# Kernel optimization log

Hardware: AMD Instinct MI355X
Metric: run time of the kernel (lower is better)

The kernel has to match this reference:

```python
import jax, jax.numpy as jnp
import numpy as np

B, NPG, F, H, C, DEG = 64, 1024, 128, 128, 10, 16   # graphs, nodes/graph, feat, hidden, classes, degree
N = B * NPG            # 65536 total nodes
E = N * DEG            # 1048576 total edges
K = 820                # ceil(0.8 * 1024) SAGPooling keep count per graph


def _glorot(key, shape):
    lim = float(np.sqrt(6.0 / (shape[0] + shape[1])))
    return jax.random.uniform(key, shape, jnp.float32, -lim, lim)


def setup_inputs() -> dict:
    key = jax.random.key(0)
    ks = jax.random.split(key, 16)
    # edges: endpoints drawn within the same graph
    gid = jnp.repeat(jnp.arange(B, dtype=jnp.int64), NPG * DEG)
    src = gid * NPG + jax.random.randint(ks[0], (E,), 0, NPG, dtype=jnp.int64)
    dst = gid * NPG + jax.random.randint(ks[1], (E,), 0, NPG, dtype=jnp.int64)
    return {
        "x": jax.random.normal(ks[2], (N, F), jnp.float32),
        "src": src,
        "dst": dst,
        # conv1: GraphConv(F, H)  (lin_rel has bias, lin_root has none)
        "W1_rel": _glorot(ks[3], (F, H)), "b1": jnp.zeros((H,), jnp.float32), "W1_root": _glorot(ks[4], (F, H)),
        # convs[0], convs[1]: GraphConv(H, H)
        "W2_rel": _glorot(ks[5], (H, H)), "b2": jnp.zeros((H,), jnp.float32), "W2_root": _glorot(ks[6], (H, H)),
        "W3_rel": _glorot(ks[7], (H, H)), "b3": jnp.zeros((H,), jnp.float32), "W3_root": _glorot(ks[8], (H, H)),
        # SAGPooling score GNN: GraphConv(H, 1)
        "Ws_rel": _glorot(ks[9], (H, 1)), "bs": jnp.zeros((1,), jnp.float32), "Ws_root": _glorot(ks[10], (H, 1)),
        # MLP head
        "Wl1": _glorot(ks[11], (3 * H, H)), "bl1": jnp.zeros((H,), jnp.float32),
        "Wl2": _glorot(ks[12], (H, C)), "bl2": jnp.zeros((C,), jnp.float32),
    }


def _mean_agg(x, src, dst, emask):
    # scatter-mean of source features onto destinations, honoring edge mask
    msg = x[src] * emask[:, None]                                   # [E, d]
    agg = jax.ops.segment_sum(msg, dst, num_segments=N)             # [N, d]
    deg = jax.ops.segment_sum(emask, dst, num_segments=N)           # [N]
    return agg / jnp.maximum(deg, 1.0)[:, None]


def _gconv(x, src, dst, emask, W_rel, b, W_root):
    # PyG GraphConv: lin_rel(mean_j x_j) + lin_root(x)
    return _mean_agg(x, src, dst, emask) @ W_rel + b + x @ W_root


def _gpool(x, nmask):
    # global_mean_pool over valid nodes of each graph
    xm = (x * nmask[:, None]).reshape(B, NPG, -1).sum(axis=1)       # [B, d]
    cnt = nmask.reshape(B, NPG).sum(axis=1)                          # [B]
    return xm / cnt[:, None]


def reference(x, src, dst,
              W1_rel, b1, W1_root, W2_rel, b2, W2_root, W3_rel, b3, W3_root,
              Ws_rel, bs, Ws_root, Wl1, bl1, Wl2, bl2):
    nmask = jnp.ones((N,), x.dtype)
    emask = jnp.ones((E,), x.dtype)

    x = jax.nn.relu(_gconv(x, src, dst, emask, W1_rel, b1, W1_root))
    xs = [_gpool(x, nmask)]

    # convs[0]
    x = jax.nn.relu(_gconv(x, src, dst, emask, W2_rel, b2, W2_root))
    xs.append(_gpool(x, nmask))

    # SAGPooling (ratio=0.8): score via GraphConv(H,1), topk per graph, gate by tanh(score)
    score = _gconv(x, src, dst, emask, Ws_rel, bs, Ws_root)[:, 0]    # [N]
    score_m = jnp.where(nmask > 0, score, -1e30)
    _, idx = jax.lax.top_k(score_m.reshape(B, NPG), K)               # [B, K]
    nmask = jnp.zeros((B, NPG), x.dtype).at[jnp.arange(B)[:, None], idx].set(1.0).reshape(-1)
    x = x * jnp.tanh(score)[:, None] * nmask[:, None]
    emask = emask * nmask[src] * nmask[dst]

    # convs[1]
    x = jax.nn.relu(_gconv(x, src, dst, emask, W3_rel, b3, W3_root))
    xs.append(_gpool(x, nmask))

    h = jnp.concatenate(xs, axis=-1)                                  # [B, 3H] JumpingKnowledge 'cat'
    h = jax.nn.relu(h @ Wl1 + bl1)                                    # dropout: eval mode -> identity
    logits = h @ Wl2 + bl2
    return jax.nn.log_softmax(logits, axis=-1)
```

## Files before the change

### kernel.cpp

```cpp
#include <hip/hip_runtime.h>
#include <hip/hip_bf16.h>

#define NN 65536
#define EE 1048576
#define BG 64
#define NPGC 1024
#define KKEEP 820

typedef unsigned short u16;
typedef unsigned int u32;
typedef __attribute__((ext_vector_type(4))) float f32x4;
typedef __attribute__((ext_vector_type(2))) float f32x2;
typedef __attribute__((ext_vector_type(8))) short bf16x8;

__device__ __forceinline__ float bfu_lo(u32 u) {
    u32 x = u << 16;
    return __builtin_bit_cast(float, x);
}
__device__ __forceinline__ float bfu_hi(u32 u) {
    u32 x = u & 0xffff0000u;
    return __builtin_bit_cast(float, x);
}
__device__ __forceinline__ u16 fbf(float f) {
    __hip_bfloat16 h = __float2bfloat16(f);
    return __builtin_bit_cast(u16, h);
}
__device__ __forceinline__ u32 pack2(float a, float b) {
    return (u32)fbf(a) | ((u32)fbf(b) << 16);
}

__global__ __launch_bounds__(1024) void csr_build_kernel(const int* __restrict__ src,
                                                         const int* __restrict__ dst,
                                                         int* __restrict__ noff,
                                                         int* __restrict__ deg,
                                                         int* __restrict__ csr) {
    __shared__ int hist[NPGC];
    __shared__ int scan[NPGC];
    int g = blockIdx.x, t = threadIdx.x;
    hist[t] = 0;
    __syncthreads();
    int ebase = g * 16384;
    for (int i = t; i < 16384; i += 1024) atomicAdd(&hist[dst[ebase + i] & 1023], 1);
    __syncthreads();
    int d = hist[t];
    scan[t] = d;
    __syncthreads();
    for (int s = 1; s < NPGC; s <<= 1) {
        int add = (t >= s) ? scan[t - s] : 0;
        __syncthreads();
        scan[t] += add;
        __syncthreads();
    }
    int excl = scan[t] - d;
    int node = g * NPGC + t;
    deg[node] = d;
    noff[node] = ebase + excl;
    hist[t] = excl;
    __syncthreads();
    for (int i = t; i < 16384; i += 1024) {
        int dl = dst[ebase + i] & 1023;
        int p = atomicAdd(&hist[dl], 1);
        csr[ebase + p] = src[ebase + i];
    }
}

__global__ void prep_w_kernel(const float* __restrict__ Wr1, const float* __restrict__ Wo1,
                              const float* __restrict__ Wr2, const float* __restrict__ Wo2,
                              const float* __restrict__ Wr3, const float* __restrict__ Wo3,
                              u16* __restrict__ WT) {
    int l = blockIdx.y;
    const float* Wrel = l == 0 ? Wr1 : (l == 1 ? Wr2 : Wr3);
    const float* Wroot = l == 0 ? Wo1 : (l == 1 ? Wo2 : Wo3);
    int idx = blockIdx.x * 256 + threadIdx.x;
    int col = idx >> 7, k = idx & 127;
    float v = (col < 128) ? Wrel[k * 128 + col] : Wroot[k * 128 + (col - 128)];
    WT[l * 32768 + idx] = fbf(v);
}

template <int MODE>
__global__ __launch_bounds__(256, 2) void gemm_kernel(const u16* __restrict__ Xb,
                                                      const float* __restrict__ Xf,
                                                      const float* __restrict__ gate,
                                                      const u16* __restrict__ WT,
                                                      u16* __restrict__ Y) {
    __shared__ u16 As[128][72];
    __shared__ u16 Bs[128][72];
    int rb = blockIdx.x * 128;
    int cb = blockIdx.y * 128;
    int tid = threadIdx.x;
    int lane = tid & 63, wid = tid >> 6;
    int wr = (wid >> 1) << 6, wc = (wid & 1) << 6;
    int lr = lane & 15, lk = (lane >> 4) << 3;
    f32x4 acc[4][4] = {};

    for (int half = 0; half < 2; ++half) {
        int k0 = half << 6;
        if (half) __syncthreads();
        for (int i = tid; i < 1024; i += 256) {
            int r = i >> 3, c = (i & 7) << 3;
            uint4 av;
            if (MODE == 0) {
                av = *reinterpret_cast<const uint4*>(Xb + (size_t)(rb + r) * 128 + k0 + c);
            } else if (MODE == 1) {
                float4 f0 = *reinterpret_cast<const float4*>(Xf + (size_t)(rb + r) * 128 + k0 + c);
                float4 f1 = *reinterpret_cast<const float4*>(Xf + (size_t)(rb + r) * 128 + k0 + c + 4);
                av.x = pack2(f0.x, f0.y);
                av.y = pack2(f0.z, f0.w);
                av.z = pack2(f1.x, f1.y);
                av.w = pack2(f1.z, f1.w);
            } else {
                float g = gate[rb + r];
                uint4 w = *reinterpret_cast<const uint4*>(Xb + (size_t)(rb + r) * 128 + k0 + c);
                av.x = pack2(bfu_lo(w.x) * g, bfu_hi(w.x) * g);
                av.y = pack2(bfu_lo(w.y) * g, bfu_hi(w.y) * g);
                av.z = pack2(bfu_lo(w.z) * g, bfu_hi(w.z) * g);
                av.w = pack2(bfu_lo(w.w) * g, bfu_hi(w.w) * g);
            }
            *reinterpret_cast<uint4*>(&As[r][c]) = av;
            *reinterpret_cast<uint4*>(&Bs[r][c]) =
                *reinterpret_cast<const uint4*>(WT + (cb + r) * 128 + k0 + c);
        }
        __syncthreads();
        for (int kk = 0; kk < 64; kk += 32) {
            bf16x8 a[4], b[4];
            for (int m = 0; m < 4; ++m)
                a[m] = *reinterpret_cast<const bf16x8*>(&As[wr + m * 16 + lr][kk + lk]);
            for (int n = 0; n < 4; ++n)
                b[n] = *reinterpret_cast<const bf16x8*>(&Bs[wc + n * 16 + lr][kk + lk]);
            for (int m = 0; m < 4; ++m)
                for (int n = 0; n < 4; ++n)
                    acc[m][n] = __builtin_amdgcn_mfma_f32_16x16x32_bf16(a[m], b[n], acc[m][n], 0, 0, 0);
        }
    }
    int orow0 = rb + wr + ((lane >> 4) << 2);
    int ocol0 = cb + wc + (lane & 15);
    for (int m = 0; m < 4; ++m)
        for (int n = 0; n < 4; ++n)
            for (int r = 0; r < 4; ++r)
                Y[(size_t)(orow0 + m * 16 + r) * 256 + ocol0 + n * 16] = fbf(acc[m][n][r]);
}

__global__ __launch_bounds__(256) void agg_kernel(const u16* __restrict__ Y,
                                                  const int* __restrict__ csr,
                                                  const int* __restrict__ noff,
                                                  const int* __restrict__ deg,
                                                  const float* __restrict__ bias,
                                                  const float* __restrict__ keep,
                                                  u16* __restrict__ outb,
                                                  const float* __restrict__ wsrel,
                                                  const float* __restrict__ wsroot,
                                                  float* __restrict__ srel,
                                                  float* __restrict__ sroot,
                                                  float* __restrict__ xsp,
                                                  int base, float invdenom) {
    __shared__ float pool[4][128];
    int blk = (blockIdx.x & 7) * 1024 + (blockIdx.x >> 3);
    int wid = threadIdx.x >> 6, lane = threadIdx.x & 63;
    int hl = lane & 31;
    int half = lane >> 5;
    int node = blk * 8 + wid * 2 + half;

    int off = noff[node], dg = deg[node];
    uint2 vr = *reinterpret_cast<const uint2*>(Y + (size_t)node * 256 + 128 + hl * 4);
    float4 bb = *reinterpret_cast<const float4*>(bias + hl * 4);

    int sid = (hl < dg) ? csr[off + hl] : 0;
    float ki = 1.f, cnt;
    if (keep) {
        ki = keep[node];
        float kw = (hl < dg) ? keep[sid] : 0.f;
#pragma unroll
        for (int d = 1; d < 32; d <<= 1) kw += __shfl_xor(kw, d, 64);
        cnt = kw;
    } else {
        cnt = (float)dg;
    }

    int dgc = dg < 32 ? dg : 32;
    int dgo = __shfl_xor(dgc, 32, 64);
    int dgmax = dgc > dgo ? dgc : dgo;
    int dgmin = dgc < dgo ? dgc : dgo;
    int hb = half << 7;

    f32x2 accL = {0.f, 0.f}, accH = {0.f, 0.f};

#define LOADG(buf, g)                                                                   \
    _Pragma("unroll") for (int j = 0; j < 8; ++j) {                                     \
        int row_ = __builtin_amdgcn_ds_bpermute(hb + ((g) * 8 + j) * 4, sid);           \
        buf[j] = *reinterpret_cast<const uint2*>(Y + (size_t)row_ * 256 + hl * 4);      \
    }
#define ACCG(buf, g)                                                                    \
    if ((g) * 8 + 8 <= dgmin) {                                                         \
        _Pragma("unroll") for (int j = 0; j < 8; ++j) {                                 \
            f32x2 lo, hi;                                                               \
            lo.x = bfu_lo(buf[j].x); lo.y = bfu_lo(buf[j].y);                           \
            hi.x = bfu_hi(buf[j].x); hi.y = bfu_hi(buf[j].y);                           \
            asm("v_pk_add_f32 %0, %1, %0" : "+v"(accL) : "v"(lo));                      \
            asm("v_pk_add_f32 %0, %1, %0" : "+v"(accH) : "v"(hi));                      \
        }                                                                               \
    } else {                                                                            \
        _Pragma("unroll") for (int j = 0; j < 8; ++j) {                                 \
            float m_ = ((g) * 8 + j < dgc) ? 1.f : 0.f;                                 \
            accL.x += m_ * bfu_lo(buf[j].x); accH.x += m_ * bfu_hi(buf[j].x);           \
            accL.y += m_ * bfu_lo(buf[j].y); accH.y += m_ * bfu_hi(buf[j].y);           \
        }                                                                               \
    }

    if (dgmax > 0) {
        uint2 va[8], vb[8];
        int ngw = (dgmax + 7) >> 3;
        LOADG(va, 0)
        int g = 0;
        for (; g + 2 < ngw; g += 2) {
            LOADG(vb, g + 1)
            ACCG(va, g)
            LOADG(va, g + 2)
            ACCG(vb, g + 1)
        }
        if (g + 1 < ngw) {
            LOADG(vb, g + 1)
            ACCG(va, g)
            ACCG(vb, g + 1)
        } else {
            ACCG(va, g)
        }
    }
#undef LOADG
#undef ACCG

    for (int e = 32; e < dg; ++e) {
        int srow = csr[off + e];
        if (keep) cnt += keep[srow];
        uint2 v = *reinterpret_cast<const uint2*>(Y + (size_t)srow * 256 + hl * 4);
        accL.x += bfu_lo(v.x); accH.x += bfu_hi(v.x);
        accL.y += bfu_lo(v.y); accH.y += bfu_hi(v.y);
    }

    float inv = 1.f / fmaxf(cnt, 1.f);
    float r0 = fmaxf(accL.x * inv + bb.x + bfu_lo(vr.x), 0.f) * ki;
    float r1 = fmaxf(accH.x * inv + bb.y + bfu_hi(vr.x), 0.f) * ki;
    float r2 = fmaxf(accL.y * inv + bb.z + bfu_lo(vr.y), 0.f) * ki;
    float r3 = fmaxf(accH.y * inv + bb.w + bfu_hi(vr.y), 0.f) * ki;

    if (outb) {
        uint2 p;
        p.x = (u32)fbf(r0) | ((u32)fbf(r1) << 16);
        p.y = (u32)fbf(r2) | ((u32)fbf(r3) << 16);
        *reinterpret_cast<uint2*>(outb + (size_t)node * 128 + hl * 4) = p;
    }

    if (srel) {
        float4 w0 = *reinterpret_cast<const float4*>(wsrel + hl * 4);
        float4 w1 = *reinterpret_cast<const float4*>(wsroot + hl * 4);
        float pr = r0 * w0.x + r1 * w0.y + r2 * w0.z + r3 * w0.w;
        float po = r0 * w1.x + r1 * w1.y + r2 * w1.z + r3 * w1.w;
#pragma unroll
        for (int d = 1; d < 32; d <<= 1) {
            pr += __shfl_xor(pr, d, 64);
            po += __shfl_xor(po, d, 64);
        }
        if (hl == 0) { srel[node] = pr; sroot[node] = po; }
    }

    float s0 = r0 + __shfl_xor(r0, 32, 64);
    float s1 = r1 + __shfl_xor(r1, 32, 64);
    float s2 = r2 + __shfl_xor(r2, 32, 64);
    float s3 = r3 + __shfl_xor(r3, 32, 64);
    if (half == 0) {
        pool[wid][hl * 4 + 0] = s0;
        pool[wid][hl * 4 + 1] = s1;
        pool[wid][hl * 4 + 2] = s2;
        pool[wid][hl * 4 + 3] = s3;
    }
    __syncthreads();
    int t = threadIdx.x;
    if (t < 128) {
        float s = pool[0][t] + pool[1][t] + pool[2][t] + pool[3][t];
        int g = blk >> 7;
        int bucket = blk & 15;
        atomicAdd(&xsp[(g * 16 + bucket) * 384 + base + t], s * invdenom);
    }
}

__global__ __launch_bounds__(1024) void topk_kernel(const float* __restrict__ srel,
                                                    const float* __restrict__ sroot,
                                                    const float* __restrict__ bs,
                                                    const int* __restrict__ csr,
                                                    const int* __restrict__ noff,
                                                    const int* __restrict__ deg,
                                                    float* __restrict__ keep,
                                                    float* __restrict__ gate) {
    __shared__ float sc[NPGC];
    __shared__ int si[NPGC];
    __shared__ float ssr[NPGC];
    int g = blockIdx.x, t = threadIdx.x;
    int node = g * NPGC + t;
    ssr[t] = srel[node];
    __syncthreads();
    int off = noff[node], dg = deg[node];
    float s = 0.f;
    for (int e = 0; e < dg; ++e) s += ssr[csr[off + e] & 1023];
    sc[t] = s / fmaxf((float)dg, 1.0f) + bs[0] + sroot[node];
    si[t] = t;
    __syncthreads();
    for (int k = 2; k <= NPGC; k <<= 1) {
        for (int j = k >> 1; j > 0; j >>= 1) {
            int ixj = t ^ j;
            if (ixj > t) {
                float a = sc[t], b = sc[ixj];
                int ai = si[t], bi = si[ixj];
                bool less = (a > b) || (a == b && ai < bi);
                bool up = ((t & k) == 0);
                if (less != up) { sc[t] = b; sc[ixj] = a; si[t] = bi; si[ixj] = ai; }
            }
            __syncthreads();
        }
    }
    int onode = g * NPGC + si[t];
    float kf = (t < KKEEP) ? 1.f : 0.f;
    keep[onode] = kf;
    gate[onode] = kf * tanhf(sc[t]);
}

__global__ __launch_bounds__(512) void mlp_kernel(const float* __restrict__ xsp,
                                                  const float* __restrict__ Wl1,
                                                  const float* __restrict__ bl1,
                                                  const float* __restrict__ Wl2,
                                                  const float* __restrict__ bl2,
                                                  float* __restrict__ out) {
    __shared__ float xsl[384];
    __shared__ float part[4][128];
    __shared__ float wl2s[1280];
    __shared__ float wred[2][10];
    __shared__ float lgs[10];
    int g = blockIdx.x, tid = threadIdx.x;
    int t = tid & 127, kg = tid >> 7;

    for (int i = tid; i < 1280; i += 512) wl2s[i] = Wl2[i];
    if (tid < 384) {
        float s = 0.f;
#pragma unroll
        for (int b = 0; b < 16; ++b) s += xsp[(g * 16 + b) * 384 + tid];
        xsl[tid] = s;
    }
    __syncthreads();

    float p = 0.f;
    int k0 = kg * 96;
#pragma unroll 8
    for (int k = 0; k < 96; ++k) p += xsl[k0 + k] * Wl1[(k0 + k) * 128 + t];
    part[kg][t] = p;
    __syncthreads();

    if (tid < 128) {
        float h = fmaxf(bl1[t] + part[0][t] + part[1][t] + part[2][t] + part[3][t], 0.f);
        float pc[10];
#pragma unroll
        for (int c = 0; c < 10; ++c) pc[c] = h * wl2s[t * 10 + c];
#pragma unroll
        for (int d = 1; d < 64; d <<= 1) {
#pragma unroll
            for (int c = 0; c < 10; ++c) pc[c] += __shfl_xor(pc[c], d, 64);
        }
        if ((t & 63) == 0) {
#pragma unroll
            for (int c = 0; c < 10; ++c) wred[t >> 6][c] = pc[c];
        }
    }
    __syncthreads();
    if (tid < 10) lgs[tid] = wred[0][tid] + wred[1][tid] + bl2[tid];
    __syncthreads();
    if (tid < 10) {
        float m = lgs[0];
#pragma unroll
        for (int c = 1; c < 10; ++c) m = fmaxf(m, lgs[c]);
        float s = 0.f;
#pragma unroll
        for (int c = 0; c < 10; ++c) s += expf(lgs[c] - m);
        out[g * 10 + tid] = lgs[tid] - m - logf(s);
    }
}

extern "C" void kernel_launch(void* const* d_in, const int* in_sizes, int n_in,
                              void* d_out, int out_size, void* d_ws, size_t ws_size,
                              hipStream_t stream) {
    const float* x       = (const float*)d_in[0];
    const int*   src     = (const int*)d_in[1];
    const int*   dst     = (const int*)d_in[2];
    const float* W1_rel  = (const float*)d_in[3];
    const float* b1      = (const float*)d_in[4];
    const float* W1_root = (const float*)d_in[5];
    const float* W2_rel  = (const float*)d_in[6];
    const float* b2      = (const float*)d_in[7];
    const float* W2_root = (const float*)d_in[8];
    const float* W3_rel  = (const float*)d_in[9];
    const float* b3      = (const float*)d_in[10];
    const float* W3_root = (const float*)d_in[11];
    const float* Ws_rel  = (const float*)d_in[12];
    const float* bs      = (const float*)d_in[13];
    const float* Ws_root = (const float*)d_in[14];
    const float* Wl1     = (const float*)d_in[15];
    const float* bl1     = (const float*)d_in[16];
    const float* Wl2     = (const float*)d_in[17];
    const float* bl2     = (const float*)d_in[18];

    char* ws = (char*)d_ws;
    size_t off = 0;
    auto alloc = [&](size_t bytes) -> void* {
        void* p = ws + off;
        off += (bytes + 255) & ~(size_t)255;
        return p;
    };
    u16*   XB    = (u16*)alloc((size_t)NN * 128 * 2);
    u16*   X2B   = (u16*)alloc((size_t)NN * 128 * 2);
    u16*   YB    = (u16*)alloc((size_t)NN * 256 * 2);
    u16*   WT    = (u16*)alloc(3 * 256 * 128 * 2);
    float* SREL  = (float*)alloc(NN * 4);
    float* SROOT = (float*)alloc(NN * 4);
    float* GATE  = (float*)alloc(NN * 4);
    float* KEEP  = (float*)alloc(NN * 4);
    int*   DEG   = (int*)alloc(NN * 4);
    int*   NOFF  = (int*)alloc(NN * 4);
    int*   CSR   = (int*)alloc((size_t)EE * 4);
    float* XSP   = (float*)alloc((size_t)BG * 16 * 384 * 4);
    (void)ws_size; (void)n_in; (void)in_sizes; (void)out_size;

    hipMemsetAsync(XSP, 0, (size_t)BG * 16 * 384 * 4, stream);

    csr_build_kernel<<<BG, 1024, 0, stream>>>(src, dst, NOFF, DEG, CSR);

    prep_w_kernel<<<dim3(128, 3), 256, 0, stream>>>(W1_rel, W1_root, W2_rel, W2_root,
                                                    W3_rel, W3_root, WT);

    gemm_kernel<1><<<dim3(NN / 128, 2), 256, 0, stream>>>(nullptr, x, nullptr, WT, YB);
    agg_kernel<<<NN / 8, 256, 0, stream>>>(YB, CSR, NOFF, DEG, b1, nullptr, XB,
                                           nullptr, nullptr, nullptr, nullptr,
                                           XSP, 0, 1.f / 1024.f);

    gemm_kernel<0><<<dim3(NN / 128, 2), 256, 0, stream>>>(XB, nullptr, nullptr, WT + 32768, YB);
    agg_kernel<<<NN / 8, 256, 0, stream>>>(YB, CSR, NOFF, DEG, b2, nullptr, X2B,
                                           Ws_rel, Ws_root, SREL, SROOT,
                                           XSP, 128, 1.f / 1024.f);

    topk_kernel<<<BG, 1024, 0, stream>>>(SREL, SROOT, bs, CSR, NOFF, DEG, KEEP, GATE);

    gemm_kernel<2><<<dim3(NN / 128, 2), 256, 0, stream>>>(X2B, nullptr, GATE, WT + 65536, YB);
    agg_kernel<<<NN / 8, 256, 0, stream>>>(YB, CSR, NOFF, DEG, b3, KEEP, nullptr,
                                           nullptr, nullptr, nullptr, nullptr,
                                           XSP, 256, 1.f / (float)KKEEP);

    mlp_kernel<<<BG, 512, 0, stream>>>(XSP, Wl1, bl1, Wl2, bl2, (float*)d_out);
}
```

Baseline: 209.7 us.

## Stage per-graph neighbor features in LDS for aggregation, one thread per node

The aggregation kernel now runs one 1024-thread block per graph and 32-feature slice. It first loads that graph's neighbor-feature slice into shared memory, then each thread gathers its node's neighbors from LDS instead of doing scattered global loads. Nodes are processed in degree-sorted order, built by a new rank step in the CSR kernel, so warps have balanced loop trip counts. Pooling becomes a deterministic in-block reduction, which removes the memset and global atomics. Score partials are kept per slice, and the kept-neighbor counts for the masked layer move into the top-k kernel. The cost is 64KB of LDS per block, which limits occupancy, plus an O(N²) rank computation per graph.

Measured after the change: 244.4 us. +16.5%, slower.

```diff
diff --git a/kernel.cpp b/kernel.cpp
--- a/kernel.cpp
+++ b/kernel.cpp
@@ -10,7 +10,6 @@
 typedef unsigned short u16;
 typedef unsigned int u32;
 typedef __attribute__((ext_vector_type(4))) float f32x4;
-typedef __attribute__((ext_vector_type(2))) float f32x2;
 typedef __attribute__((ext_vector_type(8))) short bf16x8;
 
 __device__ __forceinline__ float bfu_lo(u32 u) {
@@ -33,7 +32,8 @@
                                                          const int* __restrict__ dst,
                                                          int* __restrict__ noff,
                                                          int* __restrict__ deg,
-                                                         int* __restrict__ csr) {
+                                                         int* __restrict__ csr,
+                                                         int* __restrict__ nord) {
     __shared__ int hist[NPGC];
     __shared__ int scan[NPGC];
     int g = blockIdx.x, t = threadIdx.x;
@@ -62,6 +62,15 @@
         int p = atomicAdd(&hist[dl], 1);
         csr[ebase + p] = src[ebase + i];
     }
+    scan[t] = d;
+    __syncthreads();
+    int pos = 0;
+#pragma unroll 4
+    for (int m = 0; m < NPGC; ++m) {
+        int dm = scan[m];
+        pos += (dm < d || (dm == d && m < t)) ? 1 : 0;
+    }
+    nord[g * NPGC + pos] = t;
 }
 
 __global__ void prep_w_kernel(const float* __restrict__ Wr1, const float* __restrict__ Wo1,
@@ -140,167 +149,146 @@
                 Y[(size_t)(orow0 + m * 16 + r) * 256 + ocol0 + n * 16] = fbf(acc[m][n][r]);
 }
 
-__global__ __launch_bounds__(256) void agg_kernel(const u16* __restrict__ Y,
-                                                  const int* __restrict__ csr,
-                                                  const int* __restrict__ noff,
-                                                  const int* __restrict__ deg,
-                                                  const float* __restrict__ bias,
-                                                  const float* __restrict__ keep,
-                                                  u16* __restrict__ outb,
-                                                  const float* __restrict__ wsrel,
-                                                  const float* __restrict__ wsroot,
-                                                  float* __restrict__ srel,
-                                                  float* __restrict__ sroot,
-                                                  float* __restrict__ xsp,
-                                                  int base, float invdenom) {
-    __shared__ float pool[4][128];
-    int blk = (blockIdx.x & 7) * 1024 + (blockIdx.x >> 3);
-    int wid = threadIdx.x >> 6, lane = threadIdx.x & 63;
-    int hl = lane & 31;
-    int half = lane >> 5;
-    int node = blk * 8 + wid * 2 + half;
-
+template <int LAYER>
+__global__ __launch_bounds__(1024, 4) void agg_kernel(const u16* __restrict__ Y,
+                                                      const int* __restrict__ csr,
+                                                      const int* __restrict__ noff,
+                                                      const int* __restrict__ deg,
+                                                      const int* __restrict__ nord,
+                                                      const float* __restrict__ bias,
+                                                      const float* __restrict__ keep,
+                                                      const float* __restrict__ cntg,
+                                                      u16* __restrict__ outb,
+                                                      const float* __restrict__ wsrel,
+                                                      const float* __restrict__ wsroot,
+                                                      float* __restrict__ srelp,
+                                                      float* __restrict__ srootp,
+                                                      float* __restrict__ xs,
+                                                      int base, float invdenom) {
+    __shared__ u32 sst[16 * 1024];
+    __shared__ float pool2[32 * 33];
+    int g = blockIdx.x >> 2, c = blockIdx.x & 3;
+    int t = threadIdx.x;
+    int nbase = g * NPGC;
+
+    {
+        const uint4* sp = reinterpret_cast<const uint4*>(Y + (size_t)(nbase + t) * 256 + c * 32);
+        uint4 q0 = sp[0], q1 = sp[1], q2 = sp[2], q3 = sp[3];
+        sst[0 * 1024 + t] = q0.x;  sst[1 * 1024 + t] = q0.y;
+        sst[2 * 1024 + t] = q0.z;  sst[3 * 1024 + t] = q0.w;
+        sst[4 * 1024 + t] = q1.x;  sst[5 * 1024 + t] = q1.y;
+        sst[6 * 1024 + t] = q1.z;  sst[7 * 1024 + t] = q1.w;
+        sst[8 * 1024 + t] = q2.x;  sst[9 * 1024 + t] = q2.y;
+        sst[10 * 1024 + t] = q2.z; sst[11 * 1024 + t] = q2.w;
+        sst[12 * 1024 + t] = q3.x; sst[13 * 1024 + t] = q3.y;
+        sst[14 * 1024 + t] = q3.z; sst[15 * 1024 + t] = q3.w;
+    }
+
+    int nloc = nord[nbase + t];
+    int node = nbase + nloc;
     int off = noff[node], dg = deg[node];
-    uint2 vr = *reinterpret_cast<const uint2*>(Y + (size_t)node * 256 + 128 + hl * 4);
-    float4 bb = *reinterpret_cast<const float4*>(bias + hl * 4);
-
-    int sid = (hl < dg) ? csr[off + hl] : 0;
     float ki = 1.f, cnt;
-    if (keep) {
+    if (LAYER == 2) {
         ki = keep[node];
-        float kw = (hl < dg) ? keep[sid] : 0.f;
-#pragma unroll
-        for (int d = 1; d < 32; d <<= 1) kw += __shfl_xor(kw, d, 64);
-        cnt = kw;
+        cnt = cntg[node];
     } else {
         cnt = (float)dg;
     }
-
-    int dgc = dg < 32 ? dg : 32;
-    int dgo = __shfl_xor(dgc, 32, 64);
-    int dgmax = dgc > dgo ? dgc : dgo;
-    int dgmin = dgc < dgo ? dgc : dgo;
-    int hb = half << 7;
-
-    f32x2 accL = {0.f, 0.f}, accH = {0.f, 0.f};
-
-#define LOADG(buf, g)                                                                   \
-    _Pragma("unroll") for (int j = 0; j < 8; ++j) {                                     \
-        int row_ = __builtin_amdgcn_ds_bpermute(hb + ((g) * 8 + j) * 4, sid);           \
-        buf[j] = *reinterpret_cast<const uint2*>(Y + (size_t)row_ * 256 + hl * 4);      \
-    }
-#define ACCG(buf, g)                                                                    \
-    if ((g) * 8 + 8 <= dgmin) {                                                         \
-        _Pragma("unroll") for (int j = 0; j < 8; ++j) {                                 \
-            f32x2 lo, hi;                                                               \
-            lo.x = bfu_lo(buf[j].x); lo.y = bfu_lo(buf[j].y);                           \
-            hi.x = bfu_hi(buf[j].x); hi.y = bfu_hi(buf[j].y);                           \
-            asm("v_pk_add_f32 %0, %1, %0" : "+v"(accL) : "v"(lo));                      \
-            asm("v_pk_add_f32 %0, %1, %0" : "+v"(accH) : "v"(hi));                      \
-        }                                                                               \
-    } else {                                                                            \
-        _Pragma("unroll") for (int j = 0; j < 8; ++j) {                                 \
-            float m_ = ((g) * 8 + j < dgc) ? 1.f : 0.f;                                 \
-            accL.x += m_ * bfu_lo(buf[j].x); accH.x += m_ * bfu_hi(buf[j].x);           \
-            accL.y += m_ * bfu_lo(buf[j].y); accH.y += m_ * bfu_hi(buf[j].y);           \
-        }                                                                               \
-    }
-
-    if (dgmax > 0) {
-        uint2 va[8], vb[8];
-        int ngw = (dgmax + 7) >> 3;
-        LOADG(va, 0)
-        int g = 0;
-        for (; g + 2 < ngw; g += 2) {
-            LOADG(vb, g + 1)
-            ACCG(va, g)
-            LOADG(va, g + 2)
-            ACCG(vb, g + 1)
-        }
-        if (g + 1 < ngw) {
-            LOADG(vb, g + 1)
-            ACCG(va, g)
-            ACCG(vb, g + 1)
-        } else {
-            ACCG(va, g)
-        }
-    }
-#undef LOADG
-#undef ACCG
-
-    for (int e = 32; e < dg; ++e) {
-        int srow = csr[off + e];
-        if (keep) cnt += keep[srow];
-        uint2 v = *reinterpret_cast<const uint2*>(Y + (size_t)srow * 256 + hl * 4);
-        accL.x += bfu_lo(v.x); accH.x += bfu_hi(v.x);
-        accL.y += bfu_lo(v.y); accH.y += bfu_hi(v.y);
-    }
-
-    float inv = 1.f / fmaxf(cnt, 1.f);
-    float r0 = fmaxf(accL.x * inv + bb.x + bfu_lo(vr.x), 0.f) * ki;
-    float r1 = fmaxf(accH.x * inv + bb.y + bfu_hi(vr.x), 0.f) * ki;
-    float r2 = fmaxf(accL.y * inv + bb.z + bfu_lo(vr.y), 0.f) * ki;
-    float r3 = fmaxf(accH.y * inv + bb.w + bfu_hi(vr.y), 0.f) * ki;
-
-    if (outb) {
-        uint2 p;
-        p.x = (u32)fbf(r0) | ((u32)fbf(r1) << 16);
-        p.y = (u32)fbf(r2) | ((u32)fbf(r3) << 16);
-        *reinterpret_cast<uint2*>(outb + (size_t)node * 128 + hl * 4) = p;
-    }
-
-    if (srel) {
-        float4 w0 = *reinterpret_cast<const float4*>(wsrel + hl * 4);
-        float4 w1 = *reinterpret_cast<const float4*>(wsroot + hl * 4);
-        float pr = r0 * w0.x + r1 * w0.y + r2 * w0.z + r3 * w0.w;
-        float po = r0 * w1.x + r1 * w1.y + r2 * w1.z + r3 * w1.w;
-#pragma unroll
-        for (int d = 1; d < 32; d <<= 1) {
-            pr += __shfl_xor(pr, d, 64);
-            po += __shfl_xor(po, d, 64);
-        }
-        if (hl == 0) { srel[node] = pr; sroot[node] = po; }
-    }
-
-    float s0 = r0 + __shfl_xor(r0, 32, 64);
-    float s1 = r1 + __shfl_xor(r1, 32, 64);
-    float s2 = r2 + __shfl_xor(r2, 32, 64);
-    float s3 = r3 + __shfl_xor(r3, 32, 64);
-    if (half == 0) {
-        pool[wid][hl * 4 + 0] = s0;
-        pool[wid][hl * 4 + 1] = s1;
-        pool[wid][hl * 4 + 2] = s2;
-        pool[wid][hl * 4 + 3] = s3;
-    }
-    __syncthreads();
-    int t = threadIdx.x;
-    if (t < 128) {
-        float s = pool[0][t] + pool[1][t] + pool[2][t] + pool[3][t];
-        int g = blk >> 7;
-        int bucket = blk & 15;
-        atomicAdd(&xsp[(g * 16 + bucket) * 384 + base + t], s * invdenom);
-    }
-}
-
-__global__ __launch_bounds__(1024) void topk_kernel(const float* __restrict__ srel,
-                                                    const float* __restrict__ sroot,
+    __syncthreads();
+
+    float accL[16] = {0.f, 0.f, 0.f, 0.f, 0.f, 0.f, 0.f, 0.f,
+                      0.f, 0.f, 0.f, 0.f, 0.f, 0.f, 0.f, 0.f};
+    float accH[16] = {0.f, 0.f, 0.f, 0.f, 0.f, 0.f, 0.f, 0.f,
+                      0.f, 0.f, 0.f, 0.f, 0.f, 0.f, 0.f, 0.f};
+    if (LAYER != 2 || ki != 0.f) {
+        int nbr = (dg > 0) ? (csr[off] & 1023) : 0;
+        for (int e = 0; e < dg; ++e) {
+            int nxt = (e + 1 < dg) ? (csr[off + e + 1] & 1023) : 0;
+#pragma unroll
+            for (int fp = 0; fp < 16; ++fp) {
+                u32 v = sst[fp * 1024 + nbr];
+                accL[fp] += bfu_lo(v);
+                accH[fp] += bfu_hi(v);
+            }
+            nbr = nxt;
+        }
+    }
+
+    float inv = ki / fmaxf(cnt, 1.f);
+    const uint4* rp = reinterpret_cast<const uint4*>(Y + (size_t)node * 256 + 128 + c * 32);
+    uint4 r0 = rp[0], r1 = rp[1], r2 = rp[2], r3 = rp[3];
+    u32 rr[16] = {r0.x, r0.y, r0.z, r0.w, r1.x, r1.y, r1.z, r1.w,
+                  r2.x, r2.y, r2.z, r2.w, r3.x, r3.y, r3.z, r3.w};
+    u32 pk[16];
+    float pr = 0.f, po = 0.f;
+#pragma unroll
+    for (int fp = 0; fp < 16; ++fp) {
+        float lo = fmaxf(accL[fp] * inv + bias[c * 32 + 2 * fp] + bfu_lo(rr[fp]), 0.f) * ki;
+        float hi = fmaxf(accH[fp] * inv + bias[c * 32 + 2 * fp + 1] + bfu_hi(rr[fp]), 0.f) * ki;
+        if (LAYER == 1) {
+            pr += lo * wsrel[c * 32 + 2 * fp] + hi * wsrel[c * 32 + 2 * fp + 1];
+            po += lo * wsroot[c * 32 + 2 * fp] + hi * wsroot[c * 32 + 2 * fp + 1];
+        }
+        pk[fp] = pack2(lo, hi);
+    }
+    if (LAYER != 2) {
+        uint4* op = reinterpret_cast<uint4*>(outb + (size_t)node * 128 + c * 32);
+        uint4 o0 = {pk[0], pk[1], pk[2], pk[3]};
+        uint4 o1 = {pk[4], pk[5], pk[6], pk[7]};
+        uint4 o2 = {pk[8], pk[9], pk[10], pk[11]};
+        uint4 o3 = {pk[12], pk[13], pk[14], pk[15]};
+        op[0] = o0; op[1] = o1; op[2] = o2; op[3] = o3;
+    }
+    if (LAYER == 1) {
+        srelp[(size_t)c * NN + node] = pr;
+        srootp[(size_t)c * NN + node] = po;
+    }
+
+    __syncthreads();
+#pragma unroll
+    for (int fp = 0; fp < 16; ++fp) sst[fp * 1024 + t] = pk[fp];
+    __syncthreads();
+
+    {
+        int f = t >> 5, sub = t & 31;
+        float s = 0.f;
+#pragma unroll 4
+        for (int k = 0; k < 32; ++k) {
+            u32 v = sst[(f >> 1) * 1024 + sub + 32 * k];
+            s += (f & 1) ? bfu_hi(v) : bfu_lo(v);
+        }
+        pool2[f * 33 + sub] = s;
+    }
+    __syncthreads();
+    if (t < 32) {
+        float s = 0.f;
+#pragma unroll 4
+        for (int sub = 0; sub < 32; ++sub) s += pool2[t * 33 + sub];
+        xs[g * 384 + base + c * 32 + t] = s * invdenom;
+    }
+}
+
+__global__ __launch_bounds__(1024) void topk_kernel(const float* __restrict__ srelp,
+                                                    const float* __restrict__ srootp,
                                                     const float* __restrict__ bs,
                                                     const int* __restrict__ csr,
                                                     const int* __restrict__ noff,
                                                     const int* __restrict__ deg,
                                                     float* __restrict__ keep,
-                                                    float* __restrict__ gate) {
+                                                    float* __restrict__ gate,
+                                                    float* __restrict__ cntg) {
     __shared__ float sc[NPGC];
     __shared__ int si[NPGC];
     __shared__ float ssr[NPGC];
     int g = blockIdx.x, t = threadIdx.x;
     int node = g * NPGC + t;
-    ssr[t] = srel[node];
+    ssr[t] = srelp[node] + srelp[NN + node] + srelp[2 * NN + node] + srelp[3 * NN + node];
+    float sroot = srootp[node] + srootp[NN + node] + srootp[2 * NN + node] + srootp[3 * NN + node];
     __syncthreads();
     int off = noff[node], dg = deg[node];
     float s = 0.f;
     for (int e = 0; e < dg; ++e) s += ssr[csr[off + e] & 1023];
-    sc[t] = s / fmaxf((float)dg, 1.0f) + bs[0] + sroot[node];
+    sc[t] = s / fmaxf((float)dg, 1.0f) + bs[0] + sroot;
     si[t] = t;
     __syncthreads();
     for (int k = 2; k <= NPGC; k <<= 1) {
@@ -316,13 +304,18 @@
             __syncthreads();
         }
     }
-    int onode = g * NPGC + si[t];
+    int oloc = si[t];
     float kf = (t < KKEEP) ? 1.f : 0.f;
-    keep[onode] = kf;
-    gate[onode] = kf * tanhf(sc[t]);
-}
-
-__global__ __launch_bounds__(512) void mlp_kernel(const float* __restrict__ xsp,
+    keep[g * NPGC + oloc] = kf;
+    gate[g * NPGC + oloc] = kf * tanhf(sc[t]);
+    ssr[oloc] = kf;
+    __syncthreads();
+    float cnt = 0.f;
+    for (int e = 0; e < dg; ++e) cnt += ssr[csr[off + e] & 1023];
+    cntg[node] = cnt;
+}
+
+__global__ __launch_bounds__(512) void mlp_kernel(const float* __restrict__ xs,
                                                   const float* __restrict__ Wl1,
                                                   const float* __restrict__ bl1,
                                                   const float* __restrict__ Wl2,
@@ -337,12 +330,7 @@
     int t = tid & 127, kg = tid >> 7;
 
     for (int i = tid; i < 1280; i += 512) wl2s[i] = Wl2[i];
-    if (tid < 384) {
-        float s = 0.f;
-#pragma unroll
-        for (int b = 0; b < 16; ++b) s += xsp[(g * 16 + b) * 384 + tid];
-        xsl[tid] = s;
-    }
+    if (tid < 384) xsl[tid] = xs[g * 384 + tid];
     __syncthreads();
 
     float p = 0.f;
@@ -411,43 +399,46 @@
         off += (bytes + 255) & ~(size_t)255;
         return p;
     };
-    u16*   XB    = (u16*)alloc((size_t)NN * 128 * 2);
-    u16*   X2B   = (u16*)alloc((size_t)NN * 128 * 2);
-    u16*   YB    = (u16*)alloc((size_t)NN * 256 * 2);
-    u16*   WT    = (u16*)alloc(3 * 256 * 128 * 2);
-    float* SREL  = (float*)alloc(NN * 4);
-    float* SROOT = (float*)alloc(NN * 4);
-    float* GATE  = (float*)alloc(NN * 4);
-    float* KEEP  = (float*)alloc(NN * 4);
-    int*   DEG   = (int*)alloc(NN * 4);
-    int*   NOFF  = (int*)alloc(NN * 4);
-    int*   CSR   = (int*)alloc((size_t)EE * 4);
-    float* XSP   = (float*)alloc((size_t)BG * 16 * 384 * 4);
+    u16*   XB     = (u16*)alloc((size_t)NN * 128 * 2);
+    u16*   X2B    = (u16*)alloc((size_t)NN * 128 * 2);
+    u16*   YB     = (u16*)alloc((size_t)NN * 256 * 2);
+    u16*   WT     = (u16*)alloc(3 * 256 * 128 * 2);
+    float* SRELP  = (float*)alloc((size_t)4 * NN * 4);
+    float* SROOTP = (float*)alloc((size_t)4 * NN * 4);
+    float* GATE   = (float*)alloc(NN * 4);
+    float* KEEP   = (float*)alloc(NN * 4);
+    float* CNT    = (float*)alloc(NN * 4);
+    int*   DEG    = (int*)alloc(NN * 4);
+    int*   NOFF   = (int*)alloc(NN * 4);
+    int*   NORD   = (int*)alloc(NN * 4);
+    int*   CSR    = (int*)alloc((size_t)EE * 4);
+    float* XS     = (float*)alloc((size_t)BG * 384 * 4);
     (void)ws_size; (void)n_in; (void)in_sizes; (void)out_size;
 
-    hipMemsetAsync(XSP, 0, (size_t)BG * 16 * 384 * 4, stream);
-
-    csr_build_kernel<<<BG, 1024, 0, stream>>>(src, dst, NOFF, DEG, CSR);
+    csr_build_kernel<<<BG, 1024, 0, stream>>>(src, dst, NOFF, DEG, CSR, NORD);
 
     prep_w_kernel<<<dim3(128, 3), 256, 0, stream>>>(W1_rel, W1_root, W2_rel, W2_root,
                                                     W3_rel, W3_root, WT);
 
     gemm_kernel<1><<<dim3(NN / 128, 2), 256, 0, stream>>>(nullptr, x, nullptr, WT, YB);
-    agg_kernel<<<NN / 8, 256, 0, stream>>>(YB, CSR, NOFF, DEG, b1, nullptr, XB,
-                                           nullptr, nullptr, nullptr, nullptr,
-                                           XSP, 0, 1.f / 1024.f);
+    agg_kernel<0><<<BG * 4, 1024, 0, stream>>>(YB, CSR, NOFF, DEG, NORD, b1,
+                                               nullptr, nullptr, XB,
+                                               nullptr, nullptr, nullptr, nullptr,
+                                               XS, 0, 1.f / 1024.f);
 
     gemm_kernel<0><<<dim3(NN / 128, 2), 256, 0, stream>>>(XB, nullptr, nullptr, WT + 32768, YB);
-    agg_kernel<<<NN / 8, 256, 0, stream>>>(YB, CSR, NOFF, DEG, b2, nullptr, X2B,
-                                           Ws_rel, Ws_root, SREL, SROOT,
-                                           XSP, 128, 1.f / 1024.f);
-
-    topk_kernel<<<BG, 1024, 0, stream>>>(SREL, SROOT, bs, CSR, NOFF, DEG, KEEP, GATE);
+    agg_kernel<1><<<BG * 4, 1024, 0, stream>>>(YB, CSR, NOFF, DEG, NORD, b2,
+                                               nullptr, nullptr, X2B,
+                                               Ws_rel, Ws_root, SRELP, SROOTP,
+                                               XS, 128, 1.f / 1024.f);
+
+    topk_kernel<<<BG, 1024, 0, stream>>>(SRELP, SROOTP, bs, CSR, NOFF, DEG, KEEP, GATE, CNT);
 
     gemm_kernel<2><<<dim3(NN / 128, 2), 256, 0, stream>>>(X2B, nullptr, GATE, WT + 65536, YB);
-    agg_kernel<<<NN / 8, 256, 0, stream>>>(YB, CSR, NOFF, DEG, b3, KEEP, nullptr,
-                                           nullptr, nullptr, nullptr, nullptr,
-                                           XSP, 256, 1.f / (float)KKEEP);
-
-    mlp_kernel<<<BG, 512, 0, stream>>>(XSP, Wl1, bl1, Wl2, bl2, (float*)d_out);
-}
+    agg_kernel<2><<<BG * 4, 1024, 0, stream>>>(YB, CSR, NOFF, DEG, NORD, b3,
+                                               KEEP, CNT, nullptr,
+                                               nullptr, nullptr, nullptr, nullptr,
+                                               XS, 256, 1.f / (float)KKEEP);
+
+    mlp_kernel<<<BG, 512, 0, stream>>>(XS, Wl1, bl1, Wl2, bl2, (float*)d_out);
+}
```
